# Optimization experiments

Hardware: AMD Instinct MI355X
Metric: run time of the kernel (lower is better)

The kernel has to match this reference:

```python
import jax, jax.numpy as jnp
import numpy as np

N_NODES = 50000
N_EDGES = 800000
NODE_DIM = 128
EDGE_DIM = 64
HID = 2 * NODE_DIM + EDGE_DIM  # 320


def setup_inputs() -> dict:
    key = jax.random.key(0)
    k1, k2, k3, k4 = jax.random.split(key, 4)
    x = jax.random.normal(k1, (N_NODES, NODE_DIM), dtype=jnp.float32)
    edge_index = jax.random.randint(k2, (2, N_EDGES), 0, N_NODES, dtype=jnp.int32)
    edge_ft = jax.random.normal(k3, (N_EDGES, EDGE_DIM), dtype=jnp.float32)
    kw1, kw2 = jax.random.split(k4)
    scale = 1.0 / np.sqrt(HID)
    W_val = jax.random.uniform(kw1, (NODE_DIM, HID), jnp.float32, -scale, scale)
    b_val = jnp.zeros((NODE_DIM,), jnp.float32)
    W_mul = jax.random.uniform(kw2, (NODE_DIM, HID), jnp.float32, -scale, scale)
    b_mul = jnp.zeros((NODE_DIM,), jnp.float32)
    return {"x": x, "edge_index": edge_index, "edge_ft": edge_ft,
            "W_val": W_val, "b_val": b_val, "W_mul": W_mul, "b_mul": b_mul}


def reference(x, edge_index, edge_ft, W_val, b_val, W_mul, b_mul):
    sender, receiver = edge_index[0], edge_index[1]
    # gather + concat: [E, 2*node_dim + edge_dim]
    c = jnp.concatenate([x[sender], x[receiver], edge_ft], axis=1)
    vals = jax.nn.softplus(c @ W_val.T + b_val)
    gate = jax.nn.sigmoid(c @ W_mul.T + b_mul)
    msg = vals * gate  # [E, node_dim]
    # scatter-sum by receiver into [N, node_dim]
    return jax.ops.segment_sum(msg, receiver, num_segments=x.shape[0])
```

## Files before the change

kernel.cpp:

```cpp
#include <hip/hip_runtime.h>
#include <hip/hip_bf16.h>

#define E_EDGES   800000
#define NN_NODES  50000
#define NODE_DIM  128
#define EDGE_DIM  64
#define KDIM      320
#define NTOT      256
#define BM        128
#define BK        64
#define THREADS   512

typedef _Float16 half8 __attribute__((ext_vector_type(8)));
typedef float    f32x4 __attribute__((ext_vector_type(4)));

__device__ __forceinline__ unsigned short f2h(float f) {
    _Float16 h = (_Float16)f;
    return __builtin_bit_cast(unsigned short, h);
}

__device__ __forceinline__ void gl_lds16(const void* g, void* l) {
    __builtin_amdgcn_global_load_lds(
        (const __attribute__((address_space(1))) unsigned int*)g,
        (__attribute__((address_space(3))) unsigned int*)l,
        16, 0, 0);
}

__global__ void cast_all_kernel(const float* __restrict__ x,
                                const float* __restrict__ wv,
                                const float* __restrict__ wm,
                                unsigned short* __restrict__ xh,
                                unsigned short* __restrict__ wc) {
    const int n4x = (NN_NODES * NODE_DIM) / 4;
    const int n4h = (NODE_DIM * KDIM) / 4;
    int i = blockIdx.x * blockDim.x + threadIdx.x;
    if (i < n4x) {
        float4 f = ((const float4*)x)[i];
        ushort4 o;
        o.x = f2h(f.x); o.y = f2h(f.y); o.z = f2h(f.z); o.w = f2h(f.w);
        ((ushort4*)xh)[i] = o;
    } else {
        int k = i - n4x;
        if (k >= 2 * n4h) return;
        const float* src = (k < n4h) ? wv : wm;
        int j = (k < n4h) ? k : k - n4h;
        float4 f = ((const float4*)src)[j];
        ushort4 o;
        o.x = f2h(f.x); o.y = f2h(f.y); o.z = f2h(f.z); o.w = f2h(f.w);
        ((ushort4*)wc)[k] = o;
    }
}

__global__ void __launch_bounds__(THREADS, 4)
cgc_main(const unsigned short* __restrict__ xh,
         const int* __restrict__ ei,
         const float* __restrict__ ef,
         const unsigned short* __restrict__ Wc,
         const float* __restrict__ bval,
         const float* __restrict__ bmul,
         float* __restrict__ out)
{
    __shared__ unsigned short As[BM * BK];
    __shared__ unsigned short Bs[NTOT * BK];
    __shared__ int sIdx[BM];
    __shared__ int rIdx[BM];

    const int tid  = threadIdx.x;
    const int e0   = blockIdx.x * BM;
    const int lane = tid & 63;
    const int wid  = tid >> 6;
    const int wm   = wid & 1;
    const int wn   = wid >> 1;
    const int q    = lane >> 4;
    const int l16  = lane & 15;

    if (tid < BM) {
        sIdx[tid] = ei[e0 + tid];
        rIdx[tid] = ei[E_EDGES + e0 + tid];
    }

    f32x4 acc[4][4];
    const f32x4 zero4 = {0.f, 0.f, 0.f, 0.f};
#pragma unroll
    for (int mt = 0; mt < 4; ++mt)
#pragma unroll
        for (int nt = 0; nt < 4; ++nt) acc[mt][nt] = zero4;

    for (int c = 0; c < 5; ++c) {
        __syncthreads();
        if (c < 4) {
            const int kcol = (c & 1) * 64;
            const int* idx = (c < 2) ? sIdx : rIdx;
#pragma unroll
            for (int i = 0; i < 2; ++i) {
                int u = tid + i * THREADS;
                int row = u >> 3, sl = u & 7;
                int sm = sl ^ (row & 7);
                int node = idx[row];
                gl_lds16(xh + (size_t)node * NODE_DIM + kcol + sm * 8, &As[u * 8]);
            }
        } else {
#pragma unroll
            for (int i = 0; i < 2; ++i) {
                int u = tid + i * THREADS;
                int row = u >> 3, sl = u & 7;
                int sm = sl ^ (row & 7);
                const float* s = ef + (size_t)(e0 + row) * EDGE_DIM + sm * 8;
                float4 f0 = ((const float4*)s)[0];
                float4 f1 = ((const float4*)s)[1];
                uint4 v;
                v.x = (unsigned)f2h(f0.x) | ((unsigned)f2h(f0.y) << 16);
                v.y = (unsigned)f2h(f0.z) | ((unsigned)f2h(f0.w) << 16);
                v.z = (unsigned)f2h(f1.x) | ((unsigned)f2h(f1.y) << 16);
                v.w = (unsigned)f2h(f1.z) | ((unsigned)f2h(f1.w) << 16);
                *(uint4*)(&As[u * 8]) = v;
            }
        }
        {
            const int kOff = c * BK;
#pragma unroll
            for (int i = 0; i < 4; ++i) {
                int u = tid + i * THREADS;
                int n = u >> 3, sl = u & 7;
                int sm = sl ^ (n & 7);
                gl_lds16(Wc + n * KDIM + kOff + sm * 8, &Bs[u * 8]);
            }
        }
        __syncthreads();
#pragma unroll
        for (int ks8 = 0; ks8 < 8; ks8 += 4) {
            half8 a[4], b[4];
#pragma unroll
            for (int mt = 0; mt < 4; ++mt) {
                int r = wm * 64 + mt * 16 + l16;
                a[mt] = *(const half8*)(&As[r * BK + (((ks8 + q) ^ (r & 7)) << 3)]);
            }
            const int nb0 = wn * 32;
            const int nbase[4] = { nb0, nb0 + 16, 128 + nb0, 128 + nb0 + 16 };
#pragma unroll
            for (int nt = 0; nt < 4; ++nt) {
                int n = nbase[nt] + l16;
                b[nt] = *(const half8*)(&Bs[n * BK + (((ks8 + q) ^ (n & 7)) << 3)]);
            }
#pragma unroll
            for (int mt = 0; mt < 4; ++mt)
#pragma unroll
                for (int nt = 0; nt < 4; ++nt)
                    acc[mt][nt] = __builtin_amdgcn_mfma_f32_16x16x32_f16(
                        a[mt], b[nt], acc[mt][nt], 0, 0, 0);
        }
    }

#pragma unroll
    for (int ct = 0; ct < 2; ++ct) {
        const int col = wn * 32 + ct * 16 + l16;
        const float bv = bval[col];
        const float bm = bmul[col];
#pragma unroll
        for (int mt = 0; mt < 4; ++mt) {
#pragma unroll
            for (int r = 0; r < 4; ++r) {
                float v = acc[mt][ct][r] + bv;
                float g = acc[mt][ct + 2][r] + bm;
                float sp  = fmaxf(v, 0.f) + __logf(1.f + __expf(-fabsf(v)));
                float sig = __builtin_amdgcn_rcpf(1.f + __expf(-g));
                float msg = sp * sig;
                int rl = wm * 64 + mt * 16 + q * 4 + r;
                int node = rIdx[rl];
                atomicAdd(out + (size_t)node * NODE_DIM + col, msg);
            }
        }
    }
}

extern "C" void kernel_launch(void* const* d_in, const int* in_sizes, int n_in,
                              void* d_out, int out_size, void* d_ws, size_t ws_size,
                              hipStream_t stream) {
    const float* x  = (const float*)d_in[0];
    const int*   ei = (const int*)d_in[1];
    const float* ef = (const float*)d_in[2];
    const float* Wv = (const float*)d_in[3];
    const float* bv = (const float*)d_in[4];
    const float* Wm = (const float*)d_in[5];
    const float* bm = (const float*)d_in[6];
    float* out = (float*)d_out;

    unsigned short* xh = (unsigned short*)d_ws;
    unsigned short* Wc = (unsigned short*)((char*)d_ws + 12800000);

    hipMemsetAsync(d_out, 0, (size_t)NN_NODES * NODE_DIM * sizeof(float), stream);

    const int n4x = (NN_NODES * NODE_DIM) / 4;
    const int n4w = (2 * NODE_DIM * KDIM) / 4;
    const int total = n4x + n4w;
    cast_all_kernel<<<(total + 255) / 256, 256, 0, stream>>>(x, Wv, Wm, xh, Wc);

    cgc_main<<<E_EDGES / BM, THREADS, 0, stream>>>(xh, ei, ef, Wc, bv, bm, out);
}
```

Before: 600.9 us.

## Sort edges by receiver into CSR and reduce messages in shared memory

Builds a receiver-sorted edge permutation on every call: a histogram kernel, a single-block scan kernel and an atomic scatter kernel. The main kernel then assigns 32 receiver nodes to each block, processes their edges in 128-edge tiles and accumulates messages into LDS with shared-memory atomics. Each output row is written once, which removes the global atomicAdd scatter and the output memset. In exchange it adds three preprocessing launches including a serial one-block scan. Per-block work is now uneven, with partially filled tiles, and the edge-feature reads are gathered through the permutation.

```diff
diff --git a/kernel.cpp b/kernel.cpp
--- a/kernel.cpp
+++ b/kernel.cpp
@@ -10,6 +10,10 @@
 #define BM        128
 #define BK        64
 #define THREADS   512
+#define NPB       32
+#define NPAD      50048
+#define NBLOCKS   1564
+#define ACCS      132
 
 typedef _Float16 half8 __attribute__((ext_vector_type(8)));
 typedef float    f32x4 __attribute__((ext_vector_type(4)));
@@ -51,6 +55,50 @@
     }
 }
 
+__global__ void hist_kernel(const int* __restrict__ ei, int* __restrict__ hist) {
+    int e = blockIdx.x * blockDim.x + threadIdx.x;
+    if (e < E_EDGES) atomicAdd(&hist[ei[E_EDGES + e]], 1);
+}
+
+__global__ void __launch_bounds__(1024)
+scan_kernel(const int* __restrict__ hist, int* __restrict__ row_ptr,
+            int* __restrict__ nxt) {
+    __shared__ int buf[1024];
+    __shared__ int carryS;
+    const int t = threadIdx.x;
+    if (t == 0) carryS = 0;
+    __syncthreads();
+    for (int base = 0; base < NPAD; base += 1024) {
+        int v = (base + t < NPAD) ? hist[base + t] : 0;
+        buf[t] = v;
+        __syncthreads();
+        for (int off = 1; off < 1024; off <<= 1) {
+            int add = (t >= off) ? buf[t - off] : 0;
+            __syncthreads();
+            buf[t] += add;
+            __syncthreads();
+        }
+        int incl = buf[t];
+        int c = carryS;
+        int excl = c + incl - v;
+        if (base + t < NPAD) { row_ptr[base + t] = excl; nxt[base + t] = excl; }
+        __syncthreads();
+        if (t == 1023) carryS = c + incl;
+        __syncthreads();
+    }
+    if (t == 0) row_ptr[NPAD] = carryS;
+}
+
+__global__ void scatter_kernel(const int* __restrict__ ei, int* __restrict__ nxt,
+                               int* __restrict__ perm) {
+    int e = blockIdx.x * blockDim.x + threadIdx.x;
+    if (e < E_EDGES) {
+        int r = ei[E_EDGES + e];
+        int pos = atomicAdd(&nxt[r], 1);
+        perm[pos] = e;
+    }
+}
+
 __global__ void __launch_bounds__(THREADS, 4)
 cgc_main(const unsigned short* __restrict__ xh,
          const int* __restrict__ ei,
@@ -58,15 +106,19 @@
          const unsigned short* __restrict__ Wc,
          const float* __restrict__ bval,
          const float* __restrict__ bmul,
+         const int* __restrict__ row_ptr,
+         const int* __restrict__ perm,
          float* __restrict__ out)
 {
     __shared__ unsigned short As[BM * BK];
     __shared__ unsigned short Bs[NTOT * BK];
-    __shared__ int sIdx[BM];
-    __shared__ int rIdx[BM];
+    __shared__ float accS[NPB * ACCS];
+    __shared__ int sE[BM];
+    __shared__ int rN[BM];
+    __shared__ int lnE[BM];
+    __shared__ int eID[BM];
 
     const int tid  = threadIdx.x;
-    const int e0   = blockIdx.x * BM;
     const int lane = tid & 63;
     const int wid  = tid >> 6;
     const int wm   = wid & 1;
@@ -74,102 +126,145 @@
     const int q    = lane >> 4;
     const int l16  = lane & 15;
 
-    if (tid < BM) {
-        sIdx[tid] = ei[e0 + tid];
-        rIdx[tid] = ei[E_EDGES + e0 + tid];
-    }
-
-    f32x4 acc[4][4];
+    const int nodeBase = blockIdx.x * NPB;
+    const int eStart = row_ptr[nodeBase];
+    const int eEnd   = row_ptr[nodeBase + NPB];
+
+#pragma unroll
+    for (int i = 0; i < 9; ++i) {
+        int u = tid + i * THREADS;
+        if (u < NPB * ACCS) accS[u] = 0.f;
+    }
+
     const f32x4 zero4 = {0.f, 0.f, 0.f, 0.f};
-#pragma unroll
-    for (int mt = 0; mt < 4; ++mt)
-#pragma unroll
-        for (int nt = 0; nt < 4; ++nt) acc[mt][nt] = zero4;
-
-    for (int c = 0; c < 5; ++c) {
+
+    for (int ec = eStart; ec < eEnd; ec += BM) {
         __syncthreads();
-        if (c < 4) {
-            const int kcol = (c & 1) * 64;
-            const int* idx = (c < 2) ? sIdx : rIdx;
-#pragma unroll
-            for (int i = 0; i < 2; ++i) {
-                int u = tid + i * THREADS;
-                int row = u >> 3, sl = u & 7;
-                int sm = sl ^ (row & 7);
-                int node = idx[row];
-                gl_lds16(xh + (size_t)node * NODE_DIM + kcol + sm * 8, &As[u * 8]);
-            }
-        } else {
-#pragma unroll
-            for (int i = 0; i < 2; ++i) {
-                int u = tid + i * THREADS;
-                int row = u >> 3, sl = u & 7;
-                int sm = sl ^ (row & 7);
-                const float* s = ef + (size_t)(e0 + row) * EDGE_DIM + sm * 8;
-                float4 f0 = ((const float4*)s)[0];
-                float4 f1 = ((const float4*)s)[1];
-                uint4 v;
-                v.x = (unsigned)f2h(f0.x) | ((unsigned)f2h(f0.y) << 16);
-                v.y = (unsigned)f2h(f0.z) | ((unsigned)f2h(f0.w) << 16);
-                v.z = (unsigned)f2h(f1.x) | ((unsigned)f2h(f1.y) << 16);
-                v.w = (unsigned)f2h(f1.z) | ((unsigned)f2h(f1.w) << 16);
-                *(uint4*)(&As[u * 8]) = v;
+        if (tid < BM) {
+            int i = ec + tid;
+            if (i < eEnd) {
+                int p = perm[i];
+                eID[tid] = p;
+                sE[tid]  = ei[p];
+                int r    = ei[E_EDGES + p];
+                rN[tid]  = r;
+                lnE[tid] = r - nodeBase;
+            } else {
+                eID[tid] = 0; sE[tid] = 0; rN[tid] = 0; lnE[tid] = -1;
             }
         }
-        {
-            const int kOff = c * BK;
-#pragma unroll
-            for (int i = 0; i < 4; ++i) {
-                int u = tid + i * THREADS;
-                int n = u >> 3, sl = u & 7;
-                int sm = sl ^ (n & 7);
-                gl_lds16(Wc + n * KDIM + kOff + sm * 8, &Bs[u * 8]);
+
+        f32x4 acc[4][4];
+#pragma unroll
+        for (int mt = 0; mt < 4; ++mt)
+#pragma unroll
+            for (int nt = 0; nt < 4; ++nt) acc[mt][nt] = zero4;
+
+        for (int c = 0; c < 5; ++c) {
+            __syncthreads();
+            if (c < 4) {
+                const int kcol = (c & 1) * 64;
+                const int* idx = (c < 2) ? sE : rN;
+#pragma unroll
+                for (int i = 0; i < 2; ++i) {
+                    int u = tid + i * THREADS;
+                    int row = u >> 3, sl = u & 7;
+                    int sm = sl ^ (row & 7);
+                    int node = idx[row];
+                    gl_lds16(xh + (size_t)node * NODE_DIM + kcol + sm * 8, &As[u * 8]);
+                }
+            } else {
+#pragma unroll
+                for (int i = 0; i < 2; ++i) {
+                    int u = tid + i * THREADS;
+                    int row = u >> 3, sl = u & 7;
+                    int sm = sl ^ (row & 7);
+                    const float* s = ef + (size_t)eID[row] * EDGE_DIM + sm * 8;
+                    float4 f0 = ((const float4*)s)[0];
+                    float4 f1 = ((const float4*)s)[1];
+                    uint4 v;
+                    v.x = (unsigned)f2h(f0.x) | ((unsigned)f2h(f0.y) << 16);
+                    v.y = (unsigned)f2h(f0.z) | ((unsigned)f2h(f0.w) << 16);
+                    v.z = (unsigned)f2h(f1.x) | ((unsigned)f2h(f1.y) << 16);
+                    v.w = (unsigned)f2h(f1.z) | ((unsigned)f2h(f1.w) << 16);
+                    *(uint4*)(&As[u * 8]) = v;
+                }
+            }
+            {
+                const int kOff = c * BK;
+#pragma unroll
+                for (int i = 0; i < 4; ++i) {
+                    int u = tid + i * THREADS;
+                    int n = u >> 3, sl = u & 7;
+                    int sm = sl ^ (n & 7);
+                    gl_lds16(Wc + n * KDIM + kOff + sm * 8, &Bs[u * 8]);
+                }
+            }
+            __syncthreads();
+#pragma unroll
+            for (int ks8 = 0; ks8 < 8; ks8 += 4) {
+                half8 a[4], b[4];
+#pragma unroll
+                for (int mt = 0; mt < 4; ++mt) {
+                    int r = wm * 64 + mt * 16 + l16;
+                    a[mt] = *(const half8*)(&As[r * BK + (((ks8 + q) ^ (r & 7)) << 3)]);
+                }
+                const int nb0 = wn * 32;
+                const int nbase[4] = { nb0, nb0 + 16, 128 + nb0, 128 + nb0 + 16 };
+#pragma unroll
+                for (int nt = 0; nt < 4; ++nt) {
+                    int n = nbase[nt] + l16;
+                    b[nt] = *(const half8*)(&Bs[n * BK + (((ks8 + q) ^ (n & 7)) << 3)]);
+                }
+#pragma unroll
+                for (int mt = 0; mt < 4; ++mt)
+#pragma unroll
+                    for (int nt = 0; nt < 4; ++nt)
+                        acc[mt][nt] = __builtin_amdgcn_mfma_f32_16x16x32_f16(
+                            a[mt], b[nt], acc[mt][nt], 0, 0, 0);
             }
         }
-        __syncthreads();
-#pragma unroll
-        for (int ks8 = 0; ks8 < 8; ks8 += 4) {
-            half8 a[4], b[4];
-#pragma unroll
-            for (int mt = 0; mt < 4; ++mt) {
-                int r = wm * 64 + mt * 16 + l16;
-                a[mt] = *(const half8*)(&As[r * BK + (((ks8 + q) ^ (r & 7)) << 3)]);
-            }
-            const int nb0 = wn * 32;
-            const int nbase[4] = { nb0, nb0 + 16, 128 + nb0, 128 + nb0 + 16 };
-#pragma unroll
-            for (int nt = 0; nt < 4; ++nt) {
-                int n = nbase[nt] + l16;
-                b[nt] = *(const half8*)(&Bs[n * BK + (((ks8 + q) ^ (n & 7)) << 3)]);
-            }
-#pragma unroll
-            for (int mt = 0; mt < 4; ++mt)
-#pragma unroll
-                for (int nt = 0; nt < 4; ++nt)
-                    acc[mt][nt] = __builtin_amdgcn_mfma_f32_16x16x32_f16(
-                        a[mt], b[nt], acc[mt][nt], 0, 0, 0);
+
+#pragma unroll
+        for (int mt = 0; mt < 4; ++mt) {
+            int ln4[4];
+#pragma unroll
+            for (int r = 0; r < 4; ++r)
+                ln4[r] = lnE[wm * 64 + mt * 16 + q * 4 + r];
+#pragma unroll
+            for (int ct = 0; ct < 2; ++ct) {
+                const int col = wn * 32 + ct * 16 + l16;
+                const float bv = bval[col];
+                const float bm = bmul[col];
+                int pln = -1;
+                float sum = 0.f;
+#pragma unroll
+                for (int r = 0; r < 4; ++r) {
+                    float v = acc[mt][ct][r] + bv;
+                    float g = acc[mt][ct + 2][r] + bm;
+                    float sp  = fmaxf(v, 0.f) + __logf(1.f + __expf(-fabsf(v)));
+                    float sig = __builtin_amdgcn_rcpf(1.f + __expf(-g));
+                    float msg = sp * sig;
+                    int ln = ln4[r];
+                    if (ln != pln) {
+                        if (pln >= 0) atomicAdd(&accS[pln * ACCS + col], sum);
+                        sum = 0.f;
+                        pln = ln;
+                    }
+                    if (ln >= 0) sum += msg;
+                }
+                if (pln >= 0) atomicAdd(&accS[pln * ACCS + col], sum);
+            }
         }
     }
 
-#pragma unroll
-    for (int ct = 0; ct < 2; ++ct) {
-        const int col = wn * 32 + ct * 16 + l16;
-        const float bv = bval[col];
-        const float bm = bmul[col];
-#pragma unroll
-        for (int mt = 0; mt < 4; ++mt) {
-#pragma unroll
-            for (int r = 0; r < 4; ++r) {
-                float v = acc[mt][ct][r] + bv;
-                float g = acc[mt][ct + 2][r] + bm;
-                float sp  = fmaxf(v, 0.f) + __logf(1.f + __expf(-fabsf(v)));
-                float sig = __builtin_amdgcn_rcpf(1.f + __expf(-g));
-                float msg = sp * sig;
-                int rl = wm * 64 + mt * 16 + q * 4 + r;
-                int node = rIdx[rl];
-                atomicAdd(out + (size_t)node * NODE_DIM + col, msg);
-            }
-        }
+    __syncthreads();
+#pragma unroll
+    for (int i = 0; i < 8; ++i) {
+        int u = tid + i * THREADS;
+        int nl = u >> 7, col = u & 127;
+        int node = nodeBase + nl;
+        if (node < NN_NODES) out[(size_t)node * NODE_DIM + col] = accS[nl * ACCS + col];
     }
 }
 
@@ -185,15 +280,24 @@
     const float* bm = (const float*)d_in[6];
     float* out = (float*)d_out;
 
-    unsigned short* xh = (unsigned short*)d_ws;
-    unsigned short* Wc = (unsigned short*)((char*)d_ws + 12800000);
-
-    hipMemsetAsync(d_out, 0, (size_t)NN_NODES * NODE_DIM * sizeof(float), stream);
+    char* w = (char*)d_ws;
+    unsigned short* xh      = (unsigned short*)(w);
+    unsigned short* Wc      = (unsigned short*)(w + 12800000);
+    int*            hist    = (int*)(w + 12963840);
+    int*            row_ptr = (int*)(w + 13164032);
+    int*            nxt     = (int*)(w + 13364288);
+    int*            perm    = (int*)(w + 13564480);
+
+    hipMemsetAsync(hist, 0, NPAD * sizeof(int), stream);
 
     const int n4x = (NN_NODES * NODE_DIM) / 4;
     const int n4w = (2 * NODE_DIM * KDIM) / 4;
-    const int total = n4x + n4w;
-    cast_all_kernel<<<(total + 255) / 256, 256, 0, stream>>>(x, Wv, Wm, xh, Wc);
-
-    cgc_main<<<E_EDGES / BM, THREADS, 0, stream>>>(xh, ei, ef, Wc, bv, bm, out);
-}
+    cast_all_kernel<<<(n4x + n4w + 255) / 256, 256, 0, stream>>>(x, Wv, Wm, xh, Wc);
+
+    hist_kernel<<<E_EDGES / 256, 256, 0, stream>>>(ei, hist);
+    scan_kernel<<<1, 1024, 0, stream>>>(hist, row_ptr, nxt);
+    scatter_kernel<<<E_EDGES / 256, 256, 0, stream>>>(ei, nxt, perm);
+
+    cgc_main<<<NBLOCKS, THREADS, 0, stream>>>(xh, ei, ef, Wc, bv, bm,
+                                              row_ptr, perm, out);
+}
```

After: 930.9 us. 54.9% more time.
